# Optimization experiments

Hardware: AMD Instinct MI355X
Metric: run time of the kernel (lower is better)

## Reference

```python
import jax, jax.numpy as jnp
import numpy as np

BS, N, M, D = 8, 2048, 64, 1024
N_WAY, N_SHOT = 64, 5


def setup_inputs() -> dict:
    key = jax.random.key(0)
    k1, k2, k3, k4, k5 = jax.random.split(key, 5)
    return {
        "prototypes": jax.random.normal(k1, (BS, M, D), dtype=jnp.float32),
        "masktypes": jax.random.uniform(k2, (BS, M, D), dtype=jnp.float32),
        "query": jax.random.normal(k3, (BS, N, D), dtype=jnp.float32),
        "support": jax.random.normal(k4, (BS, N_WAY * N_SHOT, D), dtype=jnp.float32),
        "support_labels": jax.random.randint(k5, (BS, N_WAY * N_SHOT), 0, N_WAY, dtype=jnp.int64),
        "scale": jnp.ones((1,), dtype=jnp.float32),
        "n_way": N_WAY,
        "n_shot": N_SHOT,
    }


def reference(prototypes, masktypes, query, support, support_labels, scale, n_way, n_shot):
    # Masked squared Euclidean distance:
    #   logits[b,n,m] = sum_d (mask[b,m,d] * (query[b,n,d] - proto[b,m,d]))^2
    # Expanded via the GEMM trick to avoid the (bs,n,m,d) intermediate:
    #   = sum_d mask^2 q^2 - 2 sum_d q (mask^2 p) + sum_d (mask p)^2
    dims = prototypes.shape[-1]
    mask2 = masktypes * masktypes                       # [b,m,d]
    q_term = jnp.einsum('bnd,bmd->bnm', query * query, mask2)
    cross = jnp.einsum('bnd,bmd->bnm', query, mask2 * prototypes)
    mp = masktypes * prototypes                         # [b,m,d]
    p_term = jnp.sum(mp * mp, axis=-1)[:, None, :]      # [b,1,m]
    logits = (q_term - 2.0 * cross + p_term) / dims     # normalize=True
    return scale * logits
```

## Files before the change

### kernel.cpp

```cpp
#include <hip/hip_runtime.h>

#define BSZ 8
#define NQ 2048
#define MP 64
#define DD 1024
#define K2ALL 2048
#define BN 16
#define LDKQ 2056
#define NSTEP 64
#define NTILES (NQ / BN)

typedef __bf16 bf16x8 __attribute__((ext_vector_type(8)));
typedef float f32x4 __attribute__((ext_vector_type(4)));
typedef unsigned short us8 __attribute__((ext_vector_type(8)));

__device__ __forceinline__ unsigned short f2bf(float f) {
    union { float f; unsigned int u; } v; v.f = f;
    unsigned int u = v.u;
    return (unsigned short)((u + 0x7FFFu + ((u >> 16) & 1u)) >> 16);
}

__global__ __launch_bounds__(256) void pack_kernel(
    const float* __restrict__ proto,
    const float* __restrict__ mask,
    unsigned short* __restrict__ Pf,
    float* __restrict__ Pterm)
{
    const int row = blockIdx.x;
    const int m = row & 63;
    const int b = row >> 6;
    const int t = threadIdx.x;

    const float4 mk = *(const float4*)(mask  + (size_t)row * DD + 4 * t);
    const float4 pr = *(const float4*)(proto + (size_t)row * DD + 4 * t);

    const float m2x = mk.x * mk.x, m2y = mk.y * mk.y,
                m2z = mk.z * mk.z, m2w = mk.w * mk.w;
    const float ax = mk.x * pr.x, ay = mk.y * pr.y,
                az = mk.z * pr.z, aw = mk.w * pr.w;
    float pacc = ax * ax + ay * ay + az * az + aw * aw;

    us8 o;
    o[0] = f2bf(m2x); o[1] = f2bf(-2.f * m2x * pr.x);
    o[2] = f2bf(m2y); o[3] = f2bf(-2.f * m2y * pr.y);
    o[4] = f2bf(m2z); o[5] = f2bf(-2.f * m2z * pr.z);
    o[6] = f2bf(m2w); o[7] = f2bf(-2.f * m2w * pr.w);

    const int mt   = m >> 4;
    const int s    = t >> 2;
    const int lane = (t & 3) * 16 + (m & 15);
    const size_t idx = ((((size_t)(b * 4 + mt)) * 64 + s) * 64 + lane) * 8;
    *(us8*)(Pf + idx) = o;

    __shared__ float red[4];
    #pragma unroll
    for (int off = 32; off > 0; off >>= 1)
        pacc += __shfl_down(pacc, off, 64);
    const int lane64 = t & 63, w = t >> 6;
    if (lane64 == 0) red[w] = pacc;
    __syncthreads();
    if (t == 0) Pterm[row] = red[0] + red[1] + red[2] + red[3];
}

__global__ __launch_bounds__(256) void proto_main_kernel(
    const float* __restrict__ query,
    const unsigned short* __restrict__ Pf,
    const float* __restrict__ Pterm,
    const float* __restrict__ scale,
    float* __restrict__ out)
{
    __shared__ unsigned short Qs[BN][LDKQ];

    const int tid = threadIdx.x;
    const int bid = blockIdx.x;
    const int b  = bid & 7;
    const int n0 = (bid >> 3) * BN;

    const int qrow = tid >> 4;
    const int qc   = tid & 15;
    const float* qptr = query + ((size_t)b * NQ + n0 + qrow) * DD + 4 * qc;

    const int lane = tid & 63;
    const int wid  = tid >> 6;
    const int lrow = lane & 15;
    const int lq   = (lane >> 4) * 8;

    const int mcol = 16 * wid + lrow;
    const unsigned short* bbase =
        Pf + (((size_t)(b * 4 + wid)) * 64) * 512 + (size_t)lane * 8;

    float4 qv[16];
    #pragma unroll
    for (int p = 0; p < 16; ++p)
        qv[p] = *(const float4*)(qptr + 64 * p);

    const float pt = Pterm[b * MP + mcol];
    const float sc = scale[0] * (1.0f / (float)DD);

    #pragma unroll
    for (int p = 0; p < 16; ++p) {
        const float4 q = qv[p];
        us8 o;
        o[0] = f2bf(q.x * q.x); o[1] = f2bf(q.x);
        o[2] = f2bf(q.y * q.y); o[3] = f2bf(q.y);
        o[4] = f2bf(q.z * q.z); o[5] = f2bf(q.z);
        o[6] = f2bf(q.w * q.w); o[7] = f2bf(q.w);
        *(us8*)(&Qs[qrow][8 * qc + 128 * p]) = o;
    }
    __syncthreads();

    f32x4 acc = (f32x4){0.f, 0.f, 0.f, 0.f};
    bf16x8 bq[8];
    #pragma unroll
    for (int i = 0; i < 8; ++i)
        bq[i] = *(const bf16x8*)(bbase + (size_t)i * 512);

    #pragma unroll
    for (int g = 0; g < NSTEP; g += 8) {
        #pragma unroll
        for (int j = 0; j < 8; ++j) {
            const bf16x8 bb = bq[j];
            if (g + 8 + j < NSTEP)
                bq[j] = *(const bf16x8*)(bbase + (size_t)(g + 8 + j) * 512);
            const bf16x8 a = *(const bf16x8*)(&Qs[lrow][32 * (g + j) + lq]);
            acc = __builtin_amdgcn_mfma_f32_16x16x32_bf16(a, bb, acc, 0, 0, 0);
        }
    }

    const size_t ob = ((size_t)b * NQ + (size_t)(n0 + (lane >> 4) * 4)) * MP + mcol;
    #pragma unroll
    for (int r = 0; r < 4; ++r)
        out[ob + (size_t)r * MP] = (acc[r] + pt) * sc;
}

extern "C" void kernel_launch(void* const* d_in, const int* in_sizes, int n_in,
                              void* d_out, int out_size, void* d_ws, size_t ws_size,
                              hipStream_t stream) {
    (void)in_sizes; (void)n_in; (void)ws_size; (void)out_size;
    const float* proto = (const float*)d_in[0];
    const float* mask  = (const float*)d_in[1];
    const float* query = (const float*)d_in[2];
    const float* scale = (const float*)d_in[5];
    float* out = (float*)d_out;

    unsigned short* Pf = (unsigned short*)d_ws;
    float* Pterm = (float*)((char*)d_ws + (size_t)BSZ * MP * K2ALL * 2);

    pack_kernel<<<dim3(BSZ * MP), dim3(256), 0, stream>>>(proto, mask, Pf, Pterm);
    proto_main_kernel<<<dim3(BSZ * NTILES), dim3(256), 0, stream>>>(
        query, Pf, Pterm, scale, out);
}
```

Baseline: 121.8 us.

## Double query tile per block and stage K through smaller shared buffer

```diff
diff --git a/kernel.cpp b/kernel.cpp
--- a/kernel.cpp
+++ b/kernel.cpp
@@ -5,8 +5,8 @@
 #define MP 64
 #define DD 1024
 #define K2ALL 2048
-#define BN 16
-#define LDKQ 2056
+#define BN 32
+#define LQS 520
 #define NSTEP 64
 #define NTILES (NQ / BN)
 
@@ -62,75 +62,93 @@
     if (t == 0) Pterm[row] = red[0] + red[1] + red[2] + red[3];
 }
 
-__global__ __launch_bounds__(256) void proto_main_kernel(
+__global__ __launch_bounds__(256, 2) void proto_main_kernel(
     const float* __restrict__ query,
     const unsigned short* __restrict__ Pf,
     const float* __restrict__ Pterm,
     const float* __restrict__ scale,
     float* __restrict__ out)
 {
-    __shared__ unsigned short Qs[BN][LDKQ];
+    __shared__ unsigned short Qs[BN][LQS];
 
     const int tid = threadIdx.x;
     const int bid = blockIdx.x;
     const int b  = bid & 7;
     const int n0 = (bid >> 3) * BN;
 
-    const int qrow = tid >> 4;
-    const int qc   = tid & 15;
-    const float* qptr = query + ((size_t)b * NQ + n0 + qrow) * DD + 4 * qc;
+    const int qr  = tid >> 3;
+    const int qc8 = tid & 7;
+    const float* qptr = query + ((size_t)b * NQ + n0 + qr) * DD + 32 * qc8;
 
     const int lane = tid & 63;
     const int wid  = tid >> 6;
     const int lrow = lane & 15;
     const int lq   = (lane >> 4) * 8;
+    const int mcol = 16 * wid + lrow;
 
-    const int mcol = 16 * wid + lrow;
     const unsigned short* bbase =
         Pf + (((size_t)(b * 4 + wid)) * 64) * 512 + (size_t)lane * 8;
 
-    float4 qv[16];
-    #pragma unroll
-    for (int p = 0; p < 16; ++p)
-        qv[p] = *(const float4*)(qptr + 64 * p);
-
-    const float pt = Pterm[b * MP + mcol];
-    const float sc = scale[0] * (1.0f / (float)DD);
-
-    #pragma unroll
-    for (int p = 0; p < 16; ++p) {
-        const float4 q = qv[p];
-        us8 o;
-        o[0] = f2bf(q.x * q.x); o[1] = f2bf(q.x);
-        o[2] = f2bf(q.y * q.y); o[3] = f2bf(q.y);
-        o[4] = f2bf(q.z * q.z); o[5] = f2bf(q.z);
-        o[6] = f2bf(q.w * q.w); o[7] = f2bf(q.w);
-        *(us8*)(&Qs[qrow][8 * qc + 128 * p]) = o;
-    }
-    __syncthreads();
-
-    f32x4 acc = (f32x4){0.f, 0.f, 0.f, 0.f};
     bf16x8 bq[8];
     #pragma unroll
     for (int i = 0; i < 8; ++i)
         bq[i] = *(const bf16x8*)(bbase + (size_t)i * 512);
 
+    float4 qv[8];
     #pragma unroll
-    for (int g = 0; g < NSTEP; g += 8) {
+    for (int p = 0; p < 8; ++p)
+        qv[p] = *(const float4*)(qptr + 4 * p);
+
+    const float pt = Pterm[b * MP + mcol];
+    const float sc = scale[0] * (1.0f / (float)DD);
+
+    f32x4 acc0 = (f32x4){0.f, 0.f, 0.f, 0.f};
+    f32x4 acc1 = (f32x4){0.f, 0.f, 0.f, 0.f};
+
+    #pragma unroll
+    for (int stage = 0; stage < 4; ++stage) {
         #pragma unroll
-        for (int j = 0; j < 8; ++j) {
-            const bf16x8 bb = bq[j];
-            if (g + 8 + j < NSTEP)
-                bq[j] = *(const bf16x8*)(bbase + (size_t)(g + 8 + j) * 512);
-            const bf16x8 a = *(const bf16x8*)(&Qs[lrow][32 * (g + j) + lq]);
-            acc = __builtin_amdgcn_mfma_f32_16x16x32_bf16(a, bb, acc, 0, 0, 0);
+        for (int p = 0; p < 8; ++p) {
+            const float4 q = qv[p];
+            us8 o;
+            o[0] = f2bf(q.x * q.x); o[1] = f2bf(q.x);
+            o[2] = f2bf(q.y * q.y); o[3] = f2bf(q.y);
+            o[4] = f2bf(q.z * q.z); o[5] = f2bf(q.z);
+            o[6] = f2bf(q.w * q.w); o[7] = f2bf(q.w);
+            *(us8*)(&Qs[qr][64 * qc8 + 8 * p]) = o;
         }
+        __syncthreads();
+
+        if (stage < 3) {
+            const float* qn = qptr + 256 * (stage + 1);
+            #pragma unroll
+            for (int p = 0; p < 8; ++p)
+                qv[p] = *(const float4*)(qn + 4 * p);
+        }
+
+        #pragma unroll
+        for (int g = 0; g < 16; ++g) {
+            const int sg = 16 * stage + g;
+            const bf16x8 bb = bq[sg & 7];
+            if (sg + 8 < NSTEP)
+                bq[sg & 7] = *(const bf16x8*)(bbase + (size_t)(sg + 8) * 512);
+            const bf16x8 a0 = *(const bf16x8*)(&Qs[lrow][32 * g + lq]);
+            const bf16x8 a1 = *(const bf16x8*)(&Qs[16 + lrow][32 * g + lq]);
+            acc0 = __builtin_amdgcn_mfma_f32_16x16x32_bf16(a0, bb, acc0, 0, 0, 0);
+            acc1 = __builtin_amdgcn_mfma_f32_16x16x32_bf16(a1, bb, acc1, 0, 0, 0);
+        }
+        if (stage < 3) __syncthreads();
     }
 
-    const size_t ob = ((size_t)b * NQ + (size_t)(n0 + (lane >> 4) * 4)) * MP + mcol;
+    const size_t ob0 =
+        ((size_t)b * NQ + (size_t)(n0 + (lane >> 4) * 4)) * MP + mcol;
     #pragma unroll
     for (int r = 0; r < 4; ++r)
-        out[ob + (size_t)r * MP] = (acc[r] + pt) * sc;
+        out[ob0 + (size_t)r * MP] = (acc0[r] + pt) * sc;
+    const size_t ob1 = ob0 + (size_t)16 * MP;
+    #pragma unroll
+    for (int r = 0; r < 4; ++r)
+        out[ob1 + (size_t)r * MP] = (acc1[r] + pt) * sc;
 }
 
 extern "C" void kernel_launch(void* const* d_in, const int* in_sizes, int n_in,
```

Result: slower. 130.2 us (+6.9%).

## Drop LDS staging; each wave computes 16 queries against all 64 prototypes

Applied to the files above, without the earlier changes.

```diff
diff --git a/kernel.cpp b/kernel.cpp
--- a/kernel.cpp
+++ b/kernel.cpp
@@ -5,14 +5,13 @@
 #define MP 64
 #define DD 1024
 #define K2ALL 2048
-#define BN 16
-#define LDKQ 2056
 #define NSTEP 64
-#define NTILES (NQ / BN)
 
 typedef __bf16 bf16x8 __attribute__((ext_vector_type(8)));
 typedef float f32x4 __attribute__((ext_vector_type(4)));
 typedef unsigned short us8 __attribute__((ext_vector_type(8)));
+
+union FragU { us8 u; bf16x8 b; };
 
 __device__ __forceinline__ unsigned short f2bf(float f) {
     union { float f; unsigned int u; } v; v.f = f;
@@ -62,75 +61,80 @@
     if (t == 0) Pterm[row] = red[0] + red[1] + red[2] + red[3];
 }
 
-__global__ __launch_bounds__(256) void proto_main_kernel(
+__global__ __launch_bounds__(256, 1) void proto_main_kernel(
     const float* __restrict__ query,
     const unsigned short* __restrict__ Pf,
     const float* __restrict__ Pterm,
     const float* __restrict__ scale,
     float* __restrict__ out)
 {
-    __shared__ unsigned short Qs[BN][LDKQ];
+    const int tid  = threadIdx.x;
+    const int bid  = blockIdx.x;
+    const int b    = bid & 7;
+    const int wid  = tid >> 6;
+    const int lane = tid & 63;
+    const int lrow = lane & 15;
+    const int quad = lane >> 4;
+    const int n0   = (bid >> 3) * 64 + wid * 16;
 
-    const int tid = threadIdx.x;
-    const int bid = blockIdx.x;
-    const int b  = bid & 7;
-    const int n0 = (bid >> 3) * BN;
+    const float* aptr = query + ((size_t)b * NQ + n0 + lrow) * DD + 4 * quad;
+    const unsigned short* bp = Pf + ((size_t)(b * 4)) * 64 * 512 + (size_t)lane * 8;
 
-    const int qrow = tid >> 4;
-    const int qc   = tid & 15;
-    const float* qptr = query + ((size_t)b * NQ + n0 + qrow) * DD + 4 * qc;
-
-    const int lane = tid & 63;
-    const int wid  = tid >> 6;
-    const int lrow = lane & 15;
-    const int lq   = (lane >> 4) * 8;
-
-    const int mcol = 16 * wid + lrow;
-    const unsigned short* bbase =
-        Pf + (((size_t)(b * 4 + wid)) * 64) * 512 + (size_t)lane * 8;
-
-    float4 qv[16];
-    #pragma unroll
-    for (int p = 0; p < 16; ++p)
-        qv[p] = *(const float4*)(qptr + 64 * p);
-
-    const float pt = Pterm[b * MP + mcol];
-    const float sc = scale[0] * (1.0f / (float)DD);
-
-    #pragma unroll
-    for (int p = 0; p < 16; ++p) {
-        const float4 q = qv[p];
-        us8 o;
-        o[0] = f2bf(q.x * q.x); o[1] = f2bf(q.x);
-        o[2] = f2bf(q.y * q.y); o[3] = f2bf(q.y);
-        o[4] = f2bf(q.z * q.z); o[5] = f2bf(q.z);
-        o[6] = f2bf(q.w * q.w); o[7] = f2bf(q.w);
-        *(us8*)(&Qs[qrow][8 * qc + 128 * p]) = o;
-    }
-    __syncthreads();
-
-    f32x4 acc = (f32x4){0.f, 0.f, 0.f, 0.f};
-    bf16x8 bq[8];
+    float4 aq[8];
     #pragma unroll
     for (int i = 0; i < 8; ++i)
-        bq[i] = *(const bf16x8*)(bbase + (size_t)i * 512);
+        aq[i] = *(const float4*)(aptr + 16 * i);
 
+    bf16x8 bq[4][4];
     #pragma unroll
+    for (int s = 0; s < 4; ++s)
+        #pragma unroll
+        for (int mt = 0; mt < 4; ++mt)
+            bq[s][mt] = *(const bf16x8*)(bp + (size_t)mt * 32768 + (size_t)s * 512);
+
+    const float sc = scale[0] * (1.0f / (float)DD);
+    float pt[4];
+    #pragma unroll
+    for (int mt = 0; mt < 4; ++mt)
+        pt[mt] = Pterm[b * MP + 16 * mt + lrow];
+
+    f32x4 acc[4];
+    acc[0] = acc[1] = acc[2] = acc[3] = (f32x4){0.f, 0.f, 0.f, 0.f};
+
     for (int g = 0; g < NSTEP; g += 8) {
         #pragma unroll
         for (int j = 0; j < 8; ++j) {
-            const bf16x8 bb = bq[j];
-            if (g + 8 + j < NSTEP)
-                bq[j] = *(const bf16x8*)(bbase + (size_t)(g + 8 + j) * 512);
-            const bf16x8 a = *(const bf16x8*)(&Qs[lrow][32 * (g + j) + lq]);
-            acc = __builtin_amdgcn_mfma_f32_16x16x32_bf16(a, bb, acc, 0, 0, 0);
+            const int s = g + j;
+            const float4 q = aq[s & 7];
+            if (s + 8 < NSTEP)
+                aq[s & 7] = *(const float4*)(aptr + 16 * (s + 8));
+
+            FragU af;
+            af.u[0] = f2bf(q.x * q.x); af.u[1] = f2bf(q.x);
+            af.u[2] = f2bf(q.y * q.y); af.u[3] = f2bf(q.y);
+            af.u[4] = f2bf(q.z * q.z); af.u[5] = f2bf(q.z);
+            af.u[6] = f2bf(q.w * q.w); af.u[7] = f2bf(q.w);
+            const bf16x8 a = af.b;
+
+            #pragma unroll
+            for (int mt = 0; mt < 4; ++mt) {
+                const bf16x8 bb = bq[s & 3][mt];
+                if (s + 4 < NSTEP)
+                    bq[s & 3][mt] = *(const bf16x8*)(
+                        bp + (size_t)mt * 32768 + (size_t)(s + 4) * 512);
+                acc[mt] = __builtin_amdgcn_mfma_f32_16x16x32_bf16(a, bb, acc[mt], 0, 0, 0);
+            }
         }
     }
 
-    const size_t ob = ((size_t)b * NQ + (size_t)(n0 + (lane >> 4) * 4)) * MP + mcol;
     #pragma unroll
-    for (int r = 0; r < 4; ++r)
-        out[ob + (size_t)r * MP] = (acc[r] + pt) * sc;
+    for (int mt = 0; mt < 4; ++mt) {
+        const size_t ob =
+            ((size_t)b * NQ + (size_t)(n0 + quad * 4)) * MP + 16 * mt + lrow;
+        #pragma unroll
+        for (int r = 0; r < 4; ++r)
+            out[ob + (size_t)r * MP] = (acc[mt][r] + pt[mt]) * sc;
+    }
 }
 
 extern "C" void kernel_launch(void* const* d_in, const int* in_sizes, int n_in,
@@ -147,6 +151,6 @@
     float* Pterm = (float*)((char*)d_ws + (size_t)BSZ * MP * K2ALL * 2);
 
     pack_kernel<<<dim3(BSZ * MP), dim3(256), 0, stream>>>(proto, mask, Pf, Pterm);
-    proto_main_kernel<<<dim3(BSZ * NTILES), dim3(256), 0, stream>>>(
+    proto_main_kernel<<<dim3(256), dim3(256), 0, stream>>>(
         query, Pf, Pterm, scale, out);
 }
```

After: 137.7 us. +13.0%, slower.
